# Optimization experiments

Measured on AMD Instinct MI355X. Metric: run time of the kernel, lower is better.

Reference implementation:

```python
import jax, jax.numpy as jnp
import numpy as np

BATCH_SIZE = 4096
NUM_CAMS = 64
D_FEAT = 512
EPS = 1e-16  # standard safe-sqrt epsilon used by utils.euclidean_distance_matrix


def setup_inputs() -> dict:
    key = jax.random.key(0)
    x = jax.random.normal(key, (BATCH_SIZE, D_FEAT), dtype=jnp.float32)
    # calc_idx: row i indexes the (frprcam-1) same-camera off-diagonal slots,
    # all rows in a block share idx = arange(frprcam-1) + block_start
    frprcam = BATCH_SIZE // NUM_CAMS
    uf = frprcam - 1
    block_start = (np.arange(BATCH_SIZE) // frprcam) * frprcam
    idxs = jnp.asarray(block_start[:, None] + np.arange(uf)[None, :], dtype=jnp.int32)
    return {"x": x, "idxs": idxs}


def _euclidean_distance_matrix(x):
    # ||xi - xj||: gram trick with zero-masking so sqrt is safe at 0
    dot = x @ x.T                                  # [B,B]
    sq = jnp.diagonal(dot)                         # [B]
    d2 = jax.nn.relu(sq[:, None] - 2.0 * dot + sq[None, :])
    zero = (d2 == 0.0).astype(x.dtype)
    return jnp.sqrt(d2 + zero * EPS) * (1.0 - zero)


def reference(x, idxs):
    bs = x.shape[0]
    dist = _euclidean_distance_matrix(x)           # [B,B]
    # drop the diagonal: flatten()[1:].view(B-1, B+1)[:, :-1] trick
    offdiag = dist.reshape(-1)[1:].reshape(bs - 1, bs + 1)[:, :-1].reshape(bs, bs - 1)
    logits = jax.nn.softmax(-offdiag, axis=1)      # [B,B-1]
    p = jnp.take_along_axis(logits, idxs, axis=1).sum(axis=1)  # [B]
    return (-jnp.log(p)).sum() / bs
```

## Files before the change

### kernel.cpp

```cpp
#include <hip/hip_runtime.h>
#include <hip/hip_bf16.h>

#define BATCH 4096
#define DFEAT 512
#define TM 128
#define TN 128
#define BK 64
#define LDK (BK + 8)

typedef __attribute__((ext_vector_type(8))) __bf16 bf16x8;
typedef __attribute__((ext_vector_type(4))) float f32x4;

__device__ inline ushort f2bf(float f) {
    uint u = __float_as_uint(f);
    uint r = (u + 0x7FFFu + ((u >> 16) & 1u)) >> 16;
    return (ushort)r;
}

__global__ __launch_bounds__(256) void prep_kernel(
        const float* __restrict__ x, ushort* __restrict__ xb,
        float* __restrict__ sqx, float* __restrict__ num, float* __restrict__ den) {
    int t = blockIdx.x * 256 + threadIdx.x;
    if (t < BATCH) { num[t] = 0.0f; den[t] = 0.0f; }
    int wid = threadIdx.x >> 6, lane = threadIdx.x & 63;
    int row = blockIdx.x * 4 + wid;
    const float* xr = x + (size_t)row * DFEAT + lane * 8;
    float4 v0 = *(const float4*)(xr);
    float4 v1 = *(const float4*)(xr + 4);
    float f[8] = {v0.x, v0.y, v0.z, v0.w, v1.x, v1.y, v1.z, v1.w};
    float s = 0.0f;
#pragma unroll
    for (int i = 0; i < 8; i++) s += f[i] * f[i];
    uint us[4];
#pragma unroll
    for (int i = 0; i < 4; i++)
        us[i] = (uint)f2bf(f[2 * i]) | ((uint)f2bf(f[2 * i + 1]) << 16);
    *(uint4*)&xb[(size_t)row * DFEAT + lane * 8] = *(uint4*)us;
#pragma unroll
    for (int m = 32; m; m >>= 1) s += __shfl_xor(s, m, 64);
    if (lane == 0) sqx[row] = s;
}

__global__ __launch_bounds__(256) void dist_kernel(
        const ushort* __restrict__ xb, const float* __restrict__ sqx,
        float* __restrict__ num, float* __restrict__ den) {
    __shared__ __align__(16) ushort As[TM][LDK];
    __shared__ __align__(16) ushort Bs[TN][LDK];
    const int rb = blockIdx.y, cb = blockIdx.x;
    const int rowbase = rb * TM, colbase = cb * TN;
    const int tid = threadIdx.x;
    const int wid = tid >> 6, lane = tid & 63;
    const int wr = wid >> 1, wc = wid & 1;
    const int l15 = lane & 15, l4 = lane >> 4;

    f32x4 acc[4][4] = {};

    for (int kb = 0; kb < DFEAT; kb += BK) {
#pragma unroll
        for (int i = 0; i < 4; i++) {
            int u = tid + i * 256;
            int r = u >> 3, c8 = (u & 7) * 8;
            *(uint4*)&As[r][c8] = *(const uint4*)&xb[(size_t)(rowbase + r) * DFEAT + kb + c8];
            *(uint4*)&Bs[r][c8] = *(const uint4*)&xb[(size_t)(colbase + r) * DFEAT + kb + c8];
        }
        __syncthreads();
#pragma unroll
        for (int kk = 0; kk < BK; kk += 32) {
            bf16x8 a[4], b[4];
#pragma unroll
            for (int mi = 0; mi < 4; mi++)
                a[mi] = *(const bf16x8*)&As[wr * 64 + mi * 16 + l15][kk + l4 * 8];
#pragma unroll
            for (int ni = 0; ni < 4; ni++)
                b[ni] = *(const bf16x8*)&Bs[wc * 64 + ni * 16 + l15][kk + l4 * 8];
#pragma unroll
            for (int mi = 0; mi < 4; mi++)
#pragma unroll
                for (int ni = 0; ni < 4; ni++)
                    acc[mi][ni] = __builtin_amdgcn_mfma_f32_16x16x32_bf16(
                        a[mi], b[ni], acc[mi][ni], 0, 0, 0);
        }
        __syncthreads();
    }

    float sj[4];
#pragma unroll
    for (int ni = 0; ni < 4; ni++) sj[ni] = sqx[colbase + wc * 64 + ni * 16 + l15];

#pragma unroll
    for (int mi = 0; mi < 4; mi++) {
#pragma unroll
        for (int r = 0; r < 4; r++) {
            const int i = rowbase + wr * 64 + mi * 16 + 4 * l4 + r;
            const float si = sqx[i];
            float np = 0.0f, dp = 0.0f;
#pragma unroll
            for (int ni = 0; ni < 4; ni++) {
                const int j = colbase + wc * 64 + ni * 16 + l15;
                float d2 = fmaxf(si + sj[ni] - 2.0f * acc[mi][ni][r], 0.0f);
                float e = (i == j) ? 0.0f : __expf(-sqrtf(d2));
                dp += e;
                np += ((i >> 6) == (j >> 6)) ? e : 0.0f;
            }
#pragma unroll
            for (int m = 1; m <= 8; m <<= 1) {
                np += __shfl_xor(np, m, 64);
                dp += __shfl_xor(dp, m, 64);
            }
            if (l15 == 0) {
                atomicAdd(&num[i], np);
                atomicAdd(&den[i], dp);
            }
        }
    }
}

__global__ __launch_bounds__(1024) void loss_kernel(
        const float* __restrict__ num, const float* __restrict__ den,
        float* __restrict__ out) {
    __shared__ float red[16];
    int tid = threadIdx.x;
    float s = 0.0f;
    for (int i = tid; i < BATCH; i += 1024)
        s += logf(den[i]) - logf(num[i]);
#pragma unroll
    for (int m = 32; m; m >>= 1) s += __shfl_xor(s, m, 64);
    int wid = tid >> 6, lane = tid & 63;
    if (lane == 0) red[wid] = s;
    __syncthreads();
    if (wid == 0) {
        s = (lane < 16) ? red[lane] : 0.0f;
#pragma unroll
        for (int m = 8; m; m >>= 1) s += __shfl_xor(s, m, 64);
        if (lane == 0) out[0] = s / (float)BATCH;
    }
}

extern "C" void kernel_launch(void* const* d_in, const int* in_sizes, int n_in,
                              void* d_out, int out_size, void* d_ws, size_t ws_size,
                              hipStream_t stream) {
    const float* x = (const float*)d_in[0];
    char* ws = (char*)d_ws;
    ushort* xb = (ushort*)ws;
    float* sqx = (float*)(ws + (size_t)BATCH * DFEAT * 2);
    float* num = sqx + BATCH;
    float* den = num + BATCH;
    float* out = (float*)d_out;

    prep_kernel<<<BATCH / 4, 256, 0, stream>>>(x, xb, sqx, num, den);
    dim3 grid(BATCH / TN, BATCH / TM);
    dist_kernel<<<grid, 256, 0, stream>>>(xb, sqx, num, den);
    loss_kernel<<<1, 1024, 0, stream>>>(num, den, out);
}
```

Measured before the change: 109.9 us.

## Exploit distance symmetry with upper-triangle tiles and direct global-to-LDS loads

The distance kernel now launches only upper-triangular tile pairs (including the diagonal). Each off-diagonal tile adds its exp terms to both row and column denominators, which roughly halves the MFMA and exp work. Tile staging switches to global_load_lds into an unpadded shared layout, which may bring LDS bank conflicts on the MFMA fragment reads. The loss reduction becomes a multi-block kernel with an atomic add into an output that prep now zeroes. More atomics and a sqrt-based index decode are added.

```diff
diff --git a/kernel.cpp b/kernel.cpp
--- a/kernel.cpp
+++ b/kernel.cpp
@@ -6,7 +6,8 @@
 #define TM 128
 #define TN 128
 #define BK 64
-#define LDK (BK + 8)
+#define NB (BATCH / TM)
+#define NPAIR (NB * (NB + 1) / 2)
 
 typedef __attribute__((ext_vector_type(8))) __bf16 bf16x8;
 typedef __attribute__((ext_vector_type(4))) float f32x4;
@@ -19,9 +20,11 @@
 
 __global__ __launch_bounds__(256) void prep_kernel(
         const float* __restrict__ x, ushort* __restrict__ xb,
-        float* __restrict__ sqx, float* __restrict__ num, float* __restrict__ den) {
+        float* __restrict__ sqx, float* __restrict__ num, float* __restrict__ den,
+        float* __restrict__ out) {
     int t = blockIdx.x * 256 + threadIdx.x;
     if (t < BATCH) { num[t] = 0.0f; den[t] = 0.0f; }
+    if (t == 0) out[0] = 0.0f;
     int wid = threadIdx.x >> 6, lane = threadIdx.x & 63;
     int row = blockIdx.x * 4 + wid;
     const float* xr = x + (size_t)row * DFEAT + lane * 8;
@@ -44,9 +47,16 @@
 __global__ __launch_bounds__(256) void dist_kernel(
         const ushort* __restrict__ xb, const float* __restrict__ sqx,
         float* __restrict__ num, float* __restrict__ den) {
-    __shared__ __align__(16) ushort As[TM][LDK];
-    __shared__ __align__(16) ushort Bs[TN][LDK];
-    const int rb = blockIdx.y, cb = blockIdx.x;
+    __shared__ __align__(16) ushort As[TM * BK];
+    __shared__ __align__(16) ushort Bs[TN * BK];
+
+    int idx = blockIdx.x;
+    float nb5 = (float)NB + 0.5f;
+    int rb = (int)(nb5 - sqrtf(nb5 * nb5 - 2.0f * (float)idx));
+    while (rb > 0 && rb * NB - rb * (rb - 1) / 2 > idx) rb--;
+    while ((rb + 1) * NB - (rb + 1) * rb / 2 <= idx) rb++;
+    int cb = rb + idx - (rb * NB - rb * (rb - 1) / 2);
+
     const int rowbase = rb * TM, colbase = cb * TN;
     const int tid = threadIdx.x;
     const int wid = tid >> 6, lane = tid & 63;
@@ -57,11 +67,19 @@
 
     for (int kb = 0; kb < DFEAT; kb += BK) {
 #pragma unroll
-        for (int i = 0; i < 4; i++) {
-            int u = tid + i * 256;
-            int r = u >> 3, c8 = (u & 7) * 8;
-            *(uint4*)&As[r][c8] = *(const uint4*)&xb[(size_t)(rowbase + r) * DFEAT + kb + c8];
-            *(uint4*)&Bs[r][c8] = *(const uint4*)&xb[(size_t)(colbase + r) * DFEAT + kb + c8];
+        for (int q = 0; q < 4; q++) {
+            int u = q * 256 + tid;
+            int r = u >> 3, c = (u & 7) * 8;
+            const ushort* ga = &xb[(size_t)(rowbase + r) * DFEAT + kb + c];
+            const ushort* gb = &xb[(size_t)(colbase + r) * DFEAT + kb + c];
+            ushort* la = &As[(q * 256 + wid * 64) * 8];
+            ushort* lb = &Bs[(q * 256 + wid * 64) * 8];
+            __builtin_amdgcn_global_load_lds(
+                (const __attribute__((address_space(1))) void*)ga,
+                (__attribute__((address_space(3))) void*)la, 16, 0, 0);
+            __builtin_amdgcn_global_load_lds(
+                (const __attribute__((address_space(1))) void*)gb,
+                (__attribute__((address_space(3))) void*)lb, 16, 0, 0);
         }
         __syncthreads();
 #pragma unroll
@@ -69,10 +87,10 @@
             bf16x8 a[4], b[4];
 #pragma unroll
             for (int mi = 0; mi < 4; mi++)
-                a[mi] = *(const bf16x8*)&As[wr * 64 + mi * 16 + l15][kk + l4 * 8];
+                a[mi] = *(const bf16x8*)&As[(wr * 64 + mi * 16 + l15) * BK + kk + l4 * 8];
 #pragma unroll
             for (int ni = 0; ni < 4; ni++)
-                b[ni] = *(const bf16x8*)&Bs[wc * 64 + ni * 16 + l15][kk + l4 * 8];
+                b[ni] = *(const bf16x8*)&Bs[(wc * 64 + ni * 16 + l15) * BK + kk + l4 * 8];
 #pragma unroll
             for (int mi = 0; mi < 4; mi++)
 #pragma unroll
@@ -87,53 +105,77 @@
 #pragma unroll
     for (int ni = 0; ni < 4; ni++) sj[ni] = sqx[colbase + wc * 64 + ni * 16 + l15];
 
+    if (rb == cb) {
 #pragma unroll
-    for (int mi = 0; mi < 4; mi++) {
+        for (int mi = 0; mi < 4; mi++) {
 #pragma unroll
-        for (int r = 0; r < 4; r++) {
-            const int i = rowbase + wr * 64 + mi * 16 + 4 * l4 + r;
-            const float si = sqx[i];
-            float np = 0.0f, dp = 0.0f;
+            for (int r = 0; r < 4; r++) {
+                const int i = rowbase + wr * 64 + mi * 16 + 4 * l4 + r;
+                const float si = sqx[i];
+                float np = 0.0f, dp = 0.0f;
 #pragma unroll
-            for (int ni = 0; ni < 4; ni++) {
-                const int j = colbase + wc * 64 + ni * 16 + l15;
-                float d2 = fmaxf(si + sj[ni] - 2.0f * acc[mi][ni][r], 0.0f);
-                float e = (i == j) ? 0.0f : __expf(-sqrtf(d2));
-                dp += e;
-                np += ((i >> 6) == (j >> 6)) ? e : 0.0f;
+                for (int ni = 0; ni < 4; ni++) {
+                    const int j = colbase + wc * 64 + ni * 16 + l15;
+                    float d2 = fmaxf(si + sj[ni] - 2.0f * acc[mi][ni][r], 0.0f);
+                    float e = (i == j) ? 0.0f : __expf(-sqrtf(d2));
+                    dp += e;
+                    np += ((i >> 6) == (j >> 6)) ? e : 0.0f;
+                }
+#pragma unroll
+                for (int m = 1; m <= 8; m <<= 1) {
+                    np += __shfl_xor(np, m, 64);
+                    dp += __shfl_xor(dp, m, 64);
+                }
+                if (l15 == 0) {
+                    atomicAdd(&num[i], np);
+                    atomicAdd(&den[i], dp);
+                }
             }
+        }
+    } else {
+        float cde[4] = {0.0f, 0.0f, 0.0f, 0.0f};
 #pragma unroll
-            for (int m = 1; m <= 8; m <<= 1) {
-                np += __shfl_xor(np, m, 64);
-                dp += __shfl_xor(dp, m, 64);
+        for (int mi = 0; mi < 4; mi++) {
+#pragma unroll
+            for (int r = 0; r < 4; r++) {
+                const int i = rowbase + wr * 64 + mi * 16 + 4 * l4 + r;
+                const float si = sqx[i];
+                float dp = 0.0f;
+#pragma unroll
+                for (int ni = 0; ni < 4; ni++) {
+                    float d2 = fmaxf(si + sj[ni] - 2.0f * acc[mi][ni][r], 0.0f);
+                    float e = __expf(-sqrtf(d2));
+                    dp += e;
+                    cde[ni] += e;
+                }
+#pragma unroll
+                for (int m = 1; m <= 8; m <<= 1) dp += __shfl_xor(dp, m, 64);
+                if (l15 == 0) atomicAdd(&den[i], dp);
             }
-            if (l15 == 0) {
-                atomicAdd(&num[i], np);
-                atomicAdd(&den[i], dp);
-            }
+        }
+#pragma unroll
+        for (int ni = 0; ni < 4; ni++) {
+            float c = cde[ni];
+            c += __shfl_xor(c, 16, 64);
+            c += __shfl_xor(c, 32, 64);
+            if (l4 == 0) atomicAdd(&den[colbase + wc * 64 + ni * 16 + l15], c);
         }
     }
 }
 
-__global__ __launch_bounds__(1024) void loss_kernel(
+__global__ __launch_bounds__(256) void loss_kernel(
         const float* __restrict__ num, const float* __restrict__ den,
         float* __restrict__ out) {
-    __shared__ float red[16];
-    int tid = threadIdx.x;
-    float s = 0.0f;
-    for (int i = tid; i < BATCH; i += 1024)
-        s += logf(den[i]) - logf(num[i]);
+    __shared__ float red[4];
+    int t = blockIdx.x * 256 + threadIdx.x;
+    float s = logf(den[t]) - logf(num[t]);
 #pragma unroll
     for (int m = 32; m; m >>= 1) s += __shfl_xor(s, m, 64);
-    int wid = tid >> 6, lane = tid & 63;
+    int wid = threadIdx.x >> 6, lane = threadIdx.x & 63;
     if (lane == 0) red[wid] = s;
     __syncthreads();
-    if (wid == 0) {
-        s = (lane < 16) ? red[lane] : 0.0f;
-#pragma unroll
-        for (int m = 8; m; m >>= 1) s += __shfl_xor(s, m, 64);
-        if (lane == 0) out[0] = s / (float)BATCH;
-    }
+    if (threadIdx.x == 0)
+        atomicAdd(out, (red[0] + red[1] + red[2] + red[3]) * (1.0f / (float)BATCH));
 }
 
 extern "C" void kernel_launch(void* const* d_in, const int* in_sizes, int n_in,
@@ -147,8 +189,7 @@
     float* den = num + BATCH;
     float* out = (float*)d_out;
 
-    prep_kernel<<<BATCH / 4, 256, 0, stream>>>(x, xb, sqx, num, den);
-    dim3 grid(BATCH / TN, BATCH / TM);
-    dist_kernel<<<grid, 256, 0, stream>>>(xb, sqx, num, den);
-    loss_kernel<<<1, 1024, 0, stream>>>(num, den, out);
+    prep_kernel<<<BATCH / 4, 256, 0, stream>>>(x, xb, sqx, num, den, out);
+    dist_kernel<<<NPAIR, 256, 0, stream>>>(xb, sqx, num, den);
+    loss_kernel<<<BATCH / 256, 256, 0, stream>>>(num, den, out);
 }
```

Measured after the change: 104.9 us. -4.5%, faster.

## Exploit distance symmetry with triangular 64x64 tiles and atomic-free partial sums

Applied to the files above, without the earlier changes.

Computes only upper-triangular 64x64 block pairs of the distance matrix and uses each tile for both row sums and, via column sums, the transposed tile. This roughly halves the MFMA and exp work. Each tile is a single wave that loads directly from global memory without LDS, and the mapping interleaves pairs across XCDs. Per-tile partial sums are written to P/Q buffers instead of atomics, and a parallel loss kernel reduces them. Risks are lower data reuse from skipping LDS, load imbalance, and a larger workspace.

```diff
diff --git a/kernel.cpp b/kernel.cpp
--- a/kernel.cpp
+++ b/kernel.cpp
@@ -3,10 +3,11 @@
 
 #define BATCH 4096
 #define DFEAT 512
-#define TM 128
-#define TN 128
-#define BK 64
-#define LDK (BK + 8)
+#define TB 64
+#define NB (BATCH / TB)
+#define NPAIR (NB * (NB + 1) / 2)
+#define NXCD 8
+#define CPX (NPAIR / NXCD)
 
 typedef __attribute__((ext_vector_type(8))) __bf16 bf16x8;
 typedef __attribute__((ext_vector_type(4))) float f32x4;
@@ -19,9 +20,8 @@
 
 __global__ __launch_bounds__(256) void prep_kernel(
         const float* __restrict__ x, ushort* __restrict__ xb,
-        float* __restrict__ sqx, float* __restrict__ num, float* __restrict__ den) {
-    int t = blockIdx.x * 256 + threadIdx.x;
-    if (t < BATCH) { num[t] = 0.0f; den[t] = 0.0f; }
+        float* __restrict__ sqx, float* __restrict__ out) {
+    if (blockIdx.x == 0 && threadIdx.x == 0) out[0] = 0.0f;
     int wid = threadIdx.x >> 6, lane = threadIdx.x & 63;
     int row = blockIdx.x * 4 + wid;
     const float* xr = x + (size_t)row * DFEAT + lane * 8;
@@ -41,99 +41,98 @@
     if (lane == 0) sqx[row] = s;
 }
 
-__global__ __launch_bounds__(256) void dist_kernel(
+__global__ __launch_bounds__(64) void dist_kernel(
         const ushort* __restrict__ xb, const float* __restrict__ sqx,
-        float* __restrict__ num, float* __restrict__ den) {
-    __shared__ __align__(16) ushort As[TM][LDK];
-    __shared__ __align__(16) ushort Bs[TN][LDK];
-    const int rb = blockIdx.y, cb = blockIdx.x;
-    const int rowbase = rb * TM, colbase = cb * TN;
-    const int tid = threadIdx.x;
-    const int wid = tid >> 6, lane = tid & 63;
-    const int wr = wid >> 1, wc = wid & 1;
+        float* __restrict__ P, float* __restrict__ Q) {
+    int bid = blockIdx.x;
+    int idx = (bid & (NXCD - 1)) * CPX + (bid >> 3);
+
+    float nb5 = (float)NB + 0.5f;
+    int rb = (int)(nb5 - sqrtf(nb5 * nb5 - 2.0f * (float)idx));
+    while (rb > 0 && rb * NB - rb * (rb - 1) / 2 > idx) rb--;
+    while ((rb + 1) * NB - (rb + 1) * rb / 2 <= idx) rb++;
+    int cb = rb + idx - (rb * NB - rb * (rb - 1) / 2);
+
+    const int rowbase = rb * TB, colbase = cb * TB;
+    const int lane = threadIdx.x;
     const int l15 = lane & 15, l4 = lane >> 4;
 
     f32x4 acc[4][4] = {};
 
-    for (int kb = 0; kb < DFEAT; kb += BK) {
+    const ushort* arow = xb + (size_t)(rowbase + l15) * DFEAT + l4 * 8;
+    const ushort* brow = xb + (size_t)(colbase + l15) * DFEAT + l4 * 8;
+
+#pragma unroll 4
+    for (int kk = 0; kk < DFEAT; kk += 32) {
+        bf16x8 a[4], b[4];
 #pragma unroll
-        for (int i = 0; i < 4; i++) {
-            int u = tid + i * 256;
-            int r = u >> 3, c8 = (u & 7) * 8;
-            *(uint4*)&As[r][c8] = *(const uint4*)&xb[(size_t)(rowbase + r) * DFEAT + kb + c8];
-            *(uint4*)&Bs[r][c8] = *(const uint4*)&xb[(size_t)(colbase + r) * DFEAT + kb + c8];
-        }
-        __syncthreads();
+        for (int mi = 0; mi < 4; mi++)
+            a[mi] = *(const bf16x8*)(arow + (size_t)mi * 16 * DFEAT + kk);
 #pragma unroll
-        for (int kk = 0; kk < BK; kk += 32) {
-            bf16x8 a[4], b[4];
+        for (int ni = 0; ni < 4; ni++)
+            b[ni] = *(const bf16x8*)(brow + (size_t)ni * 16 * DFEAT + kk);
 #pragma unroll
-            for (int mi = 0; mi < 4; mi++)
-                a[mi] = *(const bf16x8*)&As[wr * 64 + mi * 16 + l15][kk + l4 * 8];
+        for (int mi = 0; mi < 4; mi++)
 #pragma unroll
             for (int ni = 0; ni < 4; ni++)
-                b[ni] = *(const bf16x8*)&Bs[wc * 64 + ni * 16 + l15][kk + l4 * 8];
-#pragma unroll
-            for (int mi = 0; mi < 4; mi++)
-#pragma unroll
-                for (int ni = 0; ni < 4; ni++)
-                    acc[mi][ni] = __builtin_amdgcn_mfma_f32_16x16x32_bf16(
-                        a[mi], b[ni], acc[mi][ni], 0, 0, 0);
-        }
-        __syncthreads();
+                acc[mi][ni] = __builtin_amdgcn_mfma_f32_16x16x32_bf16(
+                    a[mi], b[ni], acc[mi][ni], 0, 0, 0);
     }
 
     float sj[4];
 #pragma unroll
-    for (int ni = 0; ni < 4; ni++) sj[ni] = sqx[colbase + wc * 64 + ni * 16 + l15];
+    for (int ni = 0; ni < 4; ni++) sj[ni] = sqx[colbase + ni * 16 + l15];
 
+    float cde[4] = {0.0f, 0.0f, 0.0f, 0.0f};
 #pragma unroll
     for (int mi = 0; mi < 4; mi++) {
 #pragma unroll
         for (int r = 0; r < 4; r++) {
-            const int i = rowbase + wr * 64 + mi * 16 + 4 * l4 + r;
+            const int i = rowbase + mi * 16 + 4 * l4 + r;
             const float si = sqx[i];
-            float np = 0.0f, dp = 0.0f;
+            float dp = 0.0f;
 #pragma unroll
             for (int ni = 0; ni < 4; ni++) {
-                const int j = colbase + wc * 64 + ni * 16 + l15;
+                const int j = colbase + ni * 16 + l15;
                 float d2 = fmaxf(si + sj[ni] - 2.0f * acc[mi][ni][r], 0.0f);
                 float e = (i == j) ? 0.0f : __expf(-sqrtf(d2));
                 dp += e;
-                np += ((i >> 6) == (j >> 6)) ? e : 0.0f;
+                cde[ni] += e;
             }
 #pragma unroll
-            for (int m = 1; m <= 8; m <<= 1) {
-                np += __shfl_xor(np, m, 64);
-                dp += __shfl_xor(dp, m, 64);
-            }
-            if (l15 == 0) {
-                atomicAdd(&num[i], np);
-                atomicAdd(&den[i], dp);
-            }
+            for (int m = 1; m <= 8; m <<= 1) dp += __shfl_xor(dp, m, 64);
+            if (l15 == 0) P[(size_t)cb * BATCH + i] = dp;
+        }
+    }
+    if (rb != cb) {
+#pragma unroll
+        for (int ni = 0; ni < 4; ni++) {
+            float c = cde[ni];
+            c += __shfl_xor(c, 16, 64);
+            c += __shfl_xor(c, 32, 64);
+            if (l4 == 0) Q[(size_t)rb * BATCH + colbase + ni * 16 + l15] = c;
         }
     }
 }
 
-__global__ __launch_bounds__(1024) void loss_kernel(
-        const float* __restrict__ num, const float* __restrict__ den,
+__global__ __launch_bounds__(256) void loss_kernel(
+        const float* __restrict__ P, const float* __restrict__ Q,
         float* __restrict__ out) {
-    __shared__ float red[16];
-    int tid = threadIdx.x;
-    float s = 0.0f;
-    for (int i = tid; i < BATCH; i += 1024)
-        s += logf(den[i]) - logf(num[i]);
+    __shared__ float red[4];
+    const int i = blockIdx.x * 256 + threadIdx.x;
+    const int p = i >> 6;
+    float den = 0.0f;
+    for (int cb = p; cb < NB; cb++) den += P[(size_t)cb * BATCH + i];
+    for (int rb = 0; rb < p; rb++) den += Q[(size_t)rb * BATCH + i];
+    const float num = P[(size_t)p * BATCH + i];
+    float s = logf(den) - logf(num);
 #pragma unroll
     for (int m = 32; m; m >>= 1) s += __shfl_xor(s, m, 64);
-    int wid = tid >> 6, lane = tid & 63;
+    int wid = threadIdx.x >> 6, lane = threadIdx.x & 63;
     if (lane == 0) red[wid] = s;
     __syncthreads();
-    if (wid == 0) {
-        s = (lane < 16) ? red[lane] : 0.0f;
-#pragma unroll
-        for (int m = 8; m; m >>= 1) s += __shfl_xor(s, m, 64);
-        if (lane == 0) out[0] = s / (float)BATCH;
-    }
+    if (threadIdx.x == 0)
+        atomicAdd(out, (red[0] + red[1] + red[2] + red[3]) * (1.0f / (float)BATCH));
 }
 
 extern "C" void kernel_launch(void* const* d_in, const int* in_sizes, int n_in,
@@ -143,12 +142,11 @@
     char* ws = (char*)d_ws;
     ushort* xb = (ushort*)ws;
     float* sqx = (float*)(ws + (size_t)BATCH * DFEAT * 2);
-    float* num = sqx + BATCH;
-    float* den = num + BATCH;
+    float* P = sqx + BATCH;
+    float* Q = P + (size_t)NB * BATCH;
     float* out = (float*)d_out;
 
-    prep_kernel<<<BATCH / 4, 256, 0, stream>>>(x, xb, sqx, num, den);
-    dim3 grid(BATCH / TN, BATCH / TM);
-    dist_kernel<<<grid, 256, 0, stream>>>(xb, sqx, num, den);
-    loss_kernel<<<1, 1024, 0, stream>>>(num, den, out);
+    prep_kernel<<<BATCH / 4, 256, 0, stream>>>(x, xb, sqx, out);
+    dist_kernel<<<NPAIR, 64, 0, stream>>>(xb, sqx, P, Q);
+    loss_kernel<<<BATCH / 256, 256, 0, stream>>>(P, Q, out);
 }
```

New measurement: 131.6 us. 19.8% more time.
